# Kernel tuning notes

Measured on AMD Instinct MI355X. Metric: run time of the kernel, lower is better.

Reference implementation:

```python
import jax, jax.numpy as jnp
import numpy as np

STRIDE = 16
HF = WF = 160
IM_H = IM_W = STRIDE * HF  # 2560
A = 15
PRE_NMS = 3000
RPN_KEEP = 300
RPN_NMS_TH = 0.7
OBJ_TH = 0.2
MIN_SIZE = 8.0
G = 7
OUT_DIM = 10
S = 2  # bilinear samples per bin per axis
NUM_FG = 3
SCORE_TH = 0.3
RCNN_NMS_TH = 0.5
FINAL_KEEP = 100
BBOX_STD = jnp.array([0.1, 0.1, 0.2, 0.2], jnp.float32)


def gen_anchors():
    base = 16.0
    anchors = []
    for r in [0.5, 1.0, 2.0]:
        for s in [2.0, 4.0, 8.0, 16.0, 32.0]:
            size = base * s
            w = size * np.sqrt(1.0 / r)
            h = size * np.sqrt(r)
            anchors.append([-w / 2, -h / 2, w / 2, h / 2])
    return jnp.asarray(np.array(anchors, np.float32))  # [A,4]


def decode_boxes(anchors, deltas):
    d = deltas * BBOX_STD
    wa = anchors[..., 2] - anchors[..., 0] + 1.0
    ha = anchors[..., 3] - anchors[..., 1] + 1.0
    cxa = anchors[..., 0] + 0.5 * wa
    cya = anchors[..., 1] + 0.5 * ha
    cx = d[..., 0] * wa + cxa
    cy = d[..., 1] * ha + cya
    w = wa * jnp.exp(jnp.minimum(d[..., 2], 4.0))
    h = ha * jnp.exp(jnp.minimum(d[..., 3], 4.0))
    boxes = jnp.stack([cx - 0.5 * w, cy - 0.5 * h, cx + 0.5 * w, cy + 0.5 * h], -1)
    hi = jnp.array([IM_W - 1.0, IM_H - 1.0, IM_W - 1.0, IM_H - 1.0], jnp.float32)
    return jnp.clip(boxes, 0.0, hi)


def greedy_nms(boxes, scores, iou_th, keep_n):
    # scores <= 0 means pre-suppressed/invalid
    N = boxes.shape[0]
    areas = jnp.maximum(boxes[:, 2] - boxes[:, 0] + 1.0, 0.0) * jnp.maximum(boxes[:, 3] - boxes[:, 1] + 1.0, 0.0)

    def body(k, st):
        sup, keep = st
        s = jnp.where(sup, -1e30, scores)
        i = jnp.argmax(s)
        valid = s[i] > -1e29
        keep = keep.at[k].set(jnp.where(valid, i.astype(jnp.int32), N))
        bi = boxes[i]
        ix1 = jnp.maximum(bi[0], boxes[:, 0]); iy1 = jnp.maximum(bi[1], boxes[:, 1])
        ix2 = jnp.minimum(bi[2], boxes[:, 2]); iy2 = jnp.minimum(bi[3], boxes[:, 3])
        inter = jnp.maximum(ix2 - ix1 + 1.0, 0.0) * jnp.maximum(iy2 - iy1 + 1.0, 0.0)
        iou = inter / jnp.maximum(areas[i] + areas - inter, 1e-6)
        sup2 = (sup | (iou > iou_th)).at[i].set(True)
        sup = jnp.where(valid, sup2, sup)
        return sup, keep

    sup0 = scores <= 0.0
    keep0 = jnp.full((keep_n,), N, jnp.int32)
    _, keep = jax.lax.fori_loop(0, keep_n, body, (sup0, keep0))
    return keep, keep < N


def rpn_proposal(rpn_cls, rpn_bbox):
    fg = rpn_cls[0, A:]                                           # [A,HF,WF] objectness
    deltas = rpn_bbox[0].reshape(A, 4, HF, WF).transpose(0, 2, 3, 1)  # [A,HF,WF,4]
    anchors = gen_anchors()
    sx = jnp.arange(WF, dtype=jnp.float32) * STRIDE
    sy = jnp.arange(HF, dtype=jnp.float32) * STRIDE
    gx, gy = jnp.meshgrid(sx, sy)                                 # [HF,WF]
    shift = jnp.stack([gx, gy, gx, gy], -1)                       # [HF,WF,4]
    all_anchors = anchors[:, None, None, :] + shift[None]         # [A,HF,WF,4]
    boxes = decode_boxes(all_anchors, deltas).reshape(-1, 4)      # [A*HF*WF,4]
    scores = fg.reshape(-1)
    w = boxes[:, 2] - boxes[:, 0] + 1.0
    h = boxes[:, 3] - boxes[:, 1] + 1.0
    ok = (w >= MIN_SIZE) & (h >= MIN_SIZE) & (scores > OBJ_TH)
    scores = jnp.where(ok, scores, 0.0)
    sc, idx = jax.lax.top_k(scores, PRE_NMS)
    bx = boxes[idx]
    keep, valid = greedy_nms(bx, sc, RPN_NMS_TH, RPN_KEEP)
    bxp = jnp.concatenate([bx, jnp.zeros((1, 4), bx.dtype)], 0)
    rois = bxp[keep] * valid[:, None].astype(bx.dtype)            # [RPN_KEEP,4]
    return rois, valid


def psroi_align(ft, rois, valid):
    # ft [490,HF,WF]; position-sensitive channel = (c*G+ph)*G+pw
    x1 = rois[:, 0] / STRIDE; y1 = rois[:, 1] / STRIDE
    x2 = rois[:, 2] / STRIDE; y2 = rois[:, 3] / STRIDE
    bw = jnp.maximum(x2 - x1, 0.1) / G
    bh = jnp.maximum(y2 - y1, 0.1) / G
    frac = (jnp.arange(S, dtype=jnp.float32) + 0.5) / S           # [S]
    grid = jnp.arange(G, dtype=jnp.float32)[None, :, None] + frac[None, None, :]  # [1,G,S]
    ys = jnp.clip(y1[:, None, None] + grid * bh[:, None, None], 0.0, HF - 1.0)    # [R,G,S]
    xs = jnp.clip(x1[:, None, None] + grid * bw[:, None, None], 0.0, WF - 1.0)
    y0 = jnp.floor(ys); x0 = jnp.floor(xs)
    wy = ys - y0; wx = xs - x0
    y0i = y0.astype(jnp.int32); x0i = x0.astype(jnp.int32)
    y1i = jnp.minimum(y0i + 1, HF - 1); x1i = jnp.minimum(x0i + 1, WF - 1)
    chan = (jnp.arange(OUT_DIM)[:, None, None] * G + jnp.arange(G)[None, :, None]) * G + jnp.arange(G)[None, None, :]
    ch = chan[None, :, :, :, None, None]                          # [1,C,G,G,1,1]
    Y0 = y0i[:, None, :, None, :, None]; Y1 = y1i[:, None, :, None, :, None]
    X0 = x0i[:, None, None, :, None, :]; X1 = x1i[:, None, None, :, None, :]
    WY = wy[:, None, :, None, :, None]; WX = wx[:, None, None, :, None, :]
    v00 = ft[ch, Y0, X0]; v01 = ft[ch, Y0, X1]
    v10 = ft[ch, Y1, X0]; v11 = ft[ch, Y1, X1]                    # [R,C,G,G,S,S]
    val = v00 * (1 - WY) * (1 - WX) + v01 * (1 - WY) * WX + v10 * WY * (1 - WX) + v11 * WY * WX
    pooled = val.mean(axis=(4, 5))                                # [R,C,G,G]
    return pooled * valid[:, None, None, None].astype(pooled.dtype)


def rcnn_proposal(cls_sm, bbox_pred, rois, valid):
    R = rois.shape[0]
    deltas = bbox_pred.reshape(R, 4, 4)[:, 1:, :]                 # [R,3,4] fg classes
    boxes = decode_boxes(rois[:, None, :], deltas)                # [R,3,4]
    scores = cls_sm[:, 1:] * valid[:, None].astype(cls_sm.dtype)  # [R,3]
    scores = jnp.where(scores > SCORE_TH, scores, 0.0)
    fb = boxes.reshape(-1, 4)
    fs = scores.reshape(-1)
    labels = jnp.tile(jnp.arange(1, NUM_FG + 1, dtype=jnp.float32), (R,))
    keep, kv = greedy_nms(fb, fs, RCNN_NMS_TH, FINAL_KEEP)
    fbp = jnp.concatenate([fb, jnp.zeros((1, 4), fb.dtype)], 0)
    fsp = jnp.concatenate([fs, jnp.zeros((1,), fs.dtype)], 0)
    flp = jnp.concatenate([labels, jnp.zeros((1,), labels.dtype)], 0)
    out = jnp.concatenate([fbp[keep], fsp[keep][:, None], flp[keep][:, None]], -1)  # [FINAL_KEEP,6]
    return out * kv[:, None].astype(out.dtype)


def setup_inputs() -> dict:
    key = jax.random.key(0)
    ks = jax.random.split(key, 9)
    return {
        'rpn_cls_prob_reshape': jax.random.uniform(ks[0], (1, 2 * A, HF, WF), jnp.float32),
        'rpn_bbox_pred': jax.random.normal(ks[1], (1, 4 * A, HF, WF), jnp.float32),
        'ft_add_left_right': jax.random.normal(ks[2], (1, OUT_DIM * G * G, HF, WF), jnp.float32),
        'w1': jax.random.normal(ks[3], (490, 2048), jnp.float32) * 0.02,
        'b1': jnp.zeros((2048,), jnp.float32),
        'w_cls': jax.random.normal(ks[4], (2048, 4), jnp.float32) * 0.02,
        'b_cls': jnp.zeros((4,), jnp.float32),
        'w_bbox': jax.random.normal(ks[5], (2048, 16), jnp.float32) * 0.02,
        'b_bbox': jnp.zeros((16,), jnp.float32),
    }


def reference(rpn_cls_prob_reshape, rpn_bbox_pred, ft_add_left_right, w1, b1, w_cls, b_cls, w_bbox, b_bbox):
    rois, valid = rpn_proposal(rpn_cls_prob_reshape, rpn_bbox_pred)
    pooled = psroi_align(ft_add_left_right[0], rois, valid)       # [R,10,7,7]
    feats = pooled.reshape(-1, OUT_DIM * G * G)                   # [R,490]
    h = jax.nn.relu(feats @ w1 + b1)
    cls_sm = jax.nn.softmax(h @ w_cls + b_cls, axis=-1)
    bbox = h @ w_bbox + b_bbox
    return rcnn_proposal(cls_sm, bbox, rois, valid)
```

## Files before the change

### kernel.cpp

```cpp
#include <hip/hip_runtime.h>
#include <stdint.h>

#define HF_ 160
#define WF_ 160
#define HFW 25600
#define A_N 15
#define NTOT 384000
#define PRE_N 3000
#define KEEP_N 300
#define FEAT_N 490
#define HID_N 2048
#define RC_N 900
#define FIN_N 100
#define TIE_CAP 1024
#define NW 47
#define NSTAGE 384
#define RNW 15
#define FC1_MT 10
#define FC1_KP 496

__constant__ float c_hw[15] = {
  22.627416997969522f, 45.254833995939045f, 90.509667991878090f, 181.01933598375618f, 362.03867196751236f,
  16.0f, 32.0f, 64.0f, 128.0f, 256.0f,
  11.313708498984761f, 22.627416997969522f, 45.254833995939045f, 90.509667991878090f, 181.01933598375618f
};
__constant__ float c_hh[15] = {
  11.313708498984761f, 22.627416997969522f, 45.254833995939045f, 90.509667991878090f, 181.01933598375618f,
  16.0f, 32.0f, 64.0f, 128.0f, 256.0f,
  22.627416997969522f, 45.254833995939045f, 90.509667991878090f, 181.01933598375618f, 362.03867196751236f
};

__device__ __forceinline__ void decode_one(
    float ax1, float ay1, float ax2, float ay2,
    float dx, float dy, float dw, float dh,
    float& ox1, float& oy1, float& ox2, float& oy2)
{
#pragma clang fp contract(off)
  float wa = (ax2 - ax1) + 1.0f;
  float ha = (ay2 - ay1) + 1.0f;
  float cxa = ax1 + 0.5f * wa;
  float cya = ay1 + 0.5f * ha;
  float d0 = dx * 0.1f;
  float d1 = dy * 0.1f;
  float d2 = dw * 0.2f;
  float d3 = dh * 0.2f;
  float cx = d0 * wa + cxa;
  float cy = d1 * ha + cya;
  float w  = wa * expf(fminf(d2, 4.0f));
  float h  = ha * expf(fminf(d3, 4.0f));
  float x1 = cx - 0.5f * w;
  float y1 = cy - 0.5f * h;
  float x2 = cx + 0.5f * w;
  float y2 = cy + 0.5f * h;
  ox1 = fminf(fmaxf(x1, 0.0f), 2559.0f);
  oy1 = fminf(fmaxf(y1, 0.0f), 2559.0f);
  ox2 = fminf(fmaxf(x2, 0.0f), 2559.0f);
  oy2 = fminf(fmaxf(y2, 0.0f), 2559.0f);
}

__device__ __forceinline__ float iou_ref(
    float ax1, float ay1, float ax2, float ay2, float areaA,
    float bx1, float by1, float bx2, float by2)
{
#pragma clang fp contract(off)
  float ix1 = fmaxf(ax1, bx1);
  float iy1 = fmaxf(ay1, by1);
  float ix2 = fminf(ax2, bx2);
  float iy2 = fminf(ay2, by2);
  float iw = fmaxf((ix2 - ix1) + 1.0f, 0.0f);
  float ih = fmaxf((iy2 - iy1) + 1.0f, 0.0f);
  float inter = iw * ih;
  float areaB = fmaxf((bx2 - bx1) + 1.0f, 0.0f) * fmaxf((by2 - by1) + 1.0f, 0.0f);
  float den = fmaxf(areaA + areaB - inter, 1e-6f);
  return inter / den;
}

__global__ void k_zero(uint32_t* __restrict__ p, int n)
{
  int i = blockIdx.x * 256 + threadIdx.x;
  if (i < n) p[i] = 0u;
}

__global__ void k_decode_score(const float* __restrict__ cls,
                               const float* __restrict__ bbox,
                               float* __restrict__ scores)
{
  int e = blockIdx.x * 256 + threadIdx.x;
  if (e >= NTOT) return;
  int a   = e / HFW;
  int rem = e - a * HFW;
  int i   = rem / WF_;
  int j   = rem - i * WF_;
  float score = cls[(A_N + a) * HFW + rem];
  float gx = (float)(j * 16);
  float gy = (float)(i * 16);
  float hw = c_hw[a], hh = c_hh[a];
  float dx = bbox[(a * 4 + 0) * HFW + rem];
  float dy = bbox[(a * 4 + 1) * HFW + rem];
  float dw = bbox[(a * 4 + 2) * HFW + rem];
  float dh = bbox[(a * 4 + 3) * HFW + rem];
  float x1, y1, x2, y2;
  decode_one(gx - hw, gy - hh, gx + hw, gy + hh, dx, dy, dw, dh, x1, y1, x2, y2);
  float bw, bh;
  {
#pragma clang fp contract(off)
    bw = (x2 - x1) + 1.0f;
    bh = (y2 - y1) + 1.0f;
  }
  bool ok = (bw >= 8.0f) && (bh >= 8.0f) && (score > 0.2f);
  scores[e] = ok ? score : 0.0f;
}

__global__ void k_hist_hi(const float* __restrict__ scores, uint32_t* __restrict__ hist)
{
  __shared__ uint32_t lh[512];
  int t = threadIdx.x;
  for (int i = t; i < 512; i += 256) lh[i] = 0u;
  __syncthreads();
  int e = blockIdx.x * 256 + t;
  if (e < NTOT) {
    float s = scores[e];
    if (s > 0.0f) {
      uint32_t b = __float_as_uint(s) >> 16;
      if (b >= 0x3E00u && b < 0x4000u) atomicAdd(&lh[b - 0x3E00u], 1u);
      else atomicAdd(&hist[b], 1u);
    }
  }
  __syncthreads();
  for (int i = t; i < 512; i += 256) {
    uint32_t v = lh[i];
    if (v) atomicAdd(&hist[0x3E00u + i], v);
  }
}

__global__ void __launch_bounds__(1024) k_findbin1(const uint32_t* __restrict__ hist,
                                                   uint32_t* __restrict__ meta)
{
  __shared__ uint32_t sfx[1024];
  __shared__ int s_chunk;
  __shared__ uint32_t s_exc;
  int t = threadIdx.x;
  if (t == 0) s_chunk = -1;
  const uint32_t* hp = hist + t * 64;
  uint32_t s = 0;
#pragma unroll
  for (int b = 0; b < 64; b++) s += hp[b];
  sfx[t] = s;
  __syncthreads();
  for (int d = 1; d < 1024; d <<= 1) {
    uint32_t v = (t + d < 1024) ? sfx[t + d] : 0u;
    __syncthreads();
    sfx[t] += v;
    __syncthreads();
  }
  uint32_t inc = sfx[t];
  uint32_t exc = (t < 1023) ? sfx[t + 1] : 0u;
  if (exc < (uint32_t)PRE_N && inc >= (uint32_t)PRE_N) { s_chunk = t; s_exc = exc; }
  __syncthreads();
  int c = s_chunk;
  if (c < 0) {
    if (t == 0) { meta[0] = 0u; meta[1] = 0u; meta[2] = 1u; }
    return;
  }
  if (t < 64) {
    uint32_t h = hist[c * 64 + t];
    uint32_t v = h;
#pragma unroll
    for (int d = 1; d < 64; d <<= 1) {
      uint32_t o = (uint32_t)__shfl_down((int)v, d);
      v += (t + d < 64) ? o : 0u;
    }
    uint32_t before = s_exc + (v - h);
    if (before < (uint32_t)PRE_N && before + h >= (uint32_t)PRE_N) {
      meta[0] = (uint32_t)(c * 64 + t);
      meta[1] = (uint32_t)PRE_N - before;
      meta[2] = 0u;
    }
  }
}

__global__ void k_hist_lo(const float* __restrict__ scores,
                          const uint32_t* __restrict__ meta,
                          uint32_t* __restrict__ hist2)
{
  if (meta[2]) return;
  uint32_t B1 = meta[0];
  int e = blockIdx.x * 256 + threadIdx.x;
  if (e >= NTOT) return;
  float s = scores[e];
  if (s <= 0.0f) return;
  uint32_t bits = __float_as_uint(s);
  if ((bits >> 16) == B1) atomicAdd(&hist2[bits & 0xFFFFu], 1u);
}

__global__ void __launch_bounds__(1024) k_findT(const uint32_t* __restrict__ hist2,
                                                uint32_t* __restrict__ meta)
{
  if (meta[2]) { if (threadIdx.x == 0) meta[3] = 0u; return; }
  __shared__ uint32_t sfx[1024];
  __shared__ int s_chunk;
  __shared__ uint32_t s_exc;
  int t = threadIdx.x;
  if (t == 0) s_chunk = -1;
  uint32_t K = meta[1];
  const uint32_t* hp = hist2 + t * 64;
  uint32_t s = 0;
#pragma unroll
  for (int b = 0; b < 64; b++) s += hp[b];
  sfx[t] = s;
  __syncthreads();
  for (int d = 1; d < 1024; d <<= 1) {
    uint32_t v = (t + d < 1024) ? sfx[t + d] : 0u;
    __syncthreads();
    sfx[t] += v;
    __syncthreads();
  }
  uint32_t inc = sfx[t];
  uint32_t exc = (t < 1023) ? sfx[t + 1] : 0u;
  if (exc < K && inc >= K) { s_chunk = t; s_exc = exc; }
  __syncthreads();
  int c = s_chunk;
  if (c < 0) { if (t == 0) meta[3] = 0u; return; }
  if (t < 64) {
    uint32_t h = hist2[c * 64 + t];
    uint32_t v = h;
#pragma unroll
    for (int d = 1; d < 64; d <<= 1) {
      uint32_t o = (uint32_t)__shfl_down((int)v, d);
      v += (t + d < 64) ? o : 0u;
    }
    uint32_t before = s_exc + (v - h);
    if (before < K && before + h >= K)
      meta[3] = (meta[0] << 16) | (uint32_t)(c * 64 + t);
  }
}

__global__ void k_compact(const float* __restrict__ scores,
                          const uint32_t* __restrict__ meta,
                          uint64_t* __restrict__ gt,
                          uint64_t* __restrict__ tie,
                          uint32_t* __restrict__ cnts)
{
  int e = blockIdx.x * 256 + threadIdx.x;
  if (e >= NTOT) return;
  float s = scores[e];
  if (s <= 0.0f) return;
  uint32_t bits = __float_as_uint(s);
  uint32_t T = meta[3];
  uint64_t key = ((uint64_t)bits << 32) | (uint32_t)(~(uint32_t)e);
  if (bits > T) {
    uint32_t p = atomicAdd(&cnts[0], 1u);
    if (p < (uint32_t)PRE_N) gt[p] = key;
  } else if (bits == T) {
    uint32_t p = atomicAdd(&cnts[1], 1u);
    if (p < (uint32_t)TIE_CAP) tie[p] = key;
  }
}

__global__ void __launch_bounds__(1024) k_sort(const uint64_t* __restrict__ gt,
                                               const uint64_t* __restrict__ tie,
                                               const uint32_t* __restrict__ cnts,
                                               int* __restrict__ top_idx)
{
  __shared__ uint64_t key[4096];
  int t = threadIdx.x;
  uint32_t ngt = min(cnts[0], (uint32_t)PRE_N);
  uint32_t nte = min(cnts[1], (uint32_t)TIE_CAP);
  for (int s = t; s < 4096; s += 1024) {
    uint64_t k = 0;
    if ((uint32_t)s < ngt) k = gt[s];
    else if ((uint32_t)s < ngt + nte) k = tie[s - ngt];
    key[s] = k;
  }
  for (unsigned size = 2; size <= 4096; size <<= 1) {
    for (unsigned stride = size >> 1; stride > 0; stride >>= 1) {
      __syncthreads();
      for (unsigned i = t; i < 4096; i += 1024) {
        unsigned p = i ^ stride;
        if (p > i) {
          bool desc = ((i & size) == 0);
          uint64_t a = key[i], b = key[p];
          if (desc ? (a < b) : (a > b)) { key[i] = b; key[p] = a; }
        }
      }
    }
  }
  __syncthreads();
  for (int s = t; s < PRE_N; s += 1024) {
    uint64_t k = key[s];
    top_idx[s] = (int)(~(uint32_t)(k & 0xFFFFFFFFull));
  }
}

__global__ void k_gather(const int* __restrict__ top_idx,
                         const float* __restrict__ bbox,
                         float* __restrict__ bxx1, float* __restrict__ bxy1,
                         float* __restrict__ bxx2, float* __restrict__ bxy2)
{
  int s = blockIdx.x * 256 + threadIdx.x;
  if (s >= PRE_N) return;
  int idx = top_idx[s];
  float x1 = 0.f, y1 = 0.f, x2 = 0.f, y2 = 0.f;
  if (idx >= 0) {
    int a   = idx / HFW;
    int rem = idx - a * HFW;
    int i   = rem / WF_;
    int j   = rem - i * WF_;
    float gx = (float)(j * 16);
    float gy = (float)(i * 16);
    float hw = c_hw[a], hh = c_hh[a];
    float dx = bbox[(a * 4 + 0) * HFW + rem];
    float dy = bbox[(a * 4 + 1) * HFW + rem];
    float dw = bbox[(a * 4 + 2) * HFW + rem];
    float dh = bbox[(a * 4 + 3) * HFW + rem];
    decode_one(gx - hw, gy - hh, gx + hw, gy + hh, dx, dy, dw, dh, x1, y1, x2, y2);
  }
  bxx1[s] = x1; bxy1[s] = y1; bxx2[s] = x2; bxy2[s] = y2;
}

__global__ void __launch_bounds__(256) k_iou_mask(
    const float* __restrict__ bxx1, const float* __restrict__ bxy1,
    const float* __restrict__ bxx2, const float* __restrict__ bxy2,
    uint64_t* __restrict__ rowmask)
{
  __shared__ float s1[PRE_N], s2[PRE_N], s3[PRE_N], s4[PRE_N];
  int t = threadIdx.x;
  for (int e = t; e < PRE_N; e += 256) {
    s1[e] = bxx1[e]; s2[e] = bxy1[e]; s3[e] = bxx2[e]; s4[e] = bxy2[e];
  }
  __syncthreads();
  int task = blockIdx.x * 256 + t;
  if (task >= PRE_N * NW) return;
  int row = task / NW;
  int w   = task - row * NW;
  float ax1 = s1[row], ay1 = s2[row], ax2 = s3[row], ay2 = s4[row];
  float areaA;
  {
#pragma clang fp contract(off)
    areaA = fmaxf((ax2 - ax1) + 1.0f, 0.0f) * fmaxf((ay2 - ay1) + 1.0f, 0.0f);
  }
  int j0 = w << 6;
  uint64_t bits = 0;
  for (int off = 0; off < 64; off++) {
    int jj = (off + t) & 63;
    int j = j0 + jj;
    if (j < PRE_N) {
      float iou = iou_ref(ax1, ay1, ax2, ay2, areaA, s1[j], s2[j], s3[j], s4[j]);
      if (iou > 0.7f) bits |= 1ull << jj;
    }
  }
  rowmask[(size_t)row * NW + w] = bits;
}

__global__ void __launch_bounds__(256) k_rpn_scan(
    const float* __restrict__ bxx1, const float* __restrict__ bxy1,
    const float* __restrict__ bxx2, const float* __restrict__ bxy2,
    const uint32_t* __restrict__ cnts,
    const uint64_t* __restrict__ rowmask,
    float* __restrict__ rois, uint32_t* __restrict__ valid)
{
  __shared__ uint64_t rowstage[NSTAGE * NW];
  __shared__ int keepIdx[KEEP_N];
  __shared__ int s_nkeep;
  int t = threadIdx.x;
  for (int e = t; e < NSTAGE * NW; e += 256) rowstage[e] = rowmask[e];
  __syncthreads();
  if (t < 64) {
    int lane = t;
    uint32_t Mp = min(cnts[0] + min(cnts[1], (uint32_t)TIE_CAP), (uint32_t)PRE_N);
    uint64_t sup = 0, cw = 0;
    int nk = 0;
    for (uint32_t i = 0; i < Mp && nk < KEEP_N; i++) {
      uint32_t b = i & 63u;
      if (((cw >> b) & 1ull) == 0ull) {
        uint64_t row = 0;
        if (lane < NW)
          row = (i < NSTAGE) ? rowstage[i * NW + lane]
                             : rowmask[(size_t)i * NW + lane];
        sup |= row;
        cw |= (uint64_t)__shfl((unsigned long long)row, (int)(i >> 6));
        if (lane == 0) keepIdx[nk] = (int)i;
        nk++;
      }
      if (b == 63u) cw = (uint64_t)__shfl((unsigned long long)sup, (int)(i >> 6) + 1);
    }
    if (lane == 0) s_nkeep = nk;
  }
  __syncthreads();
  int nk2 = s_nkeep;
  for (int k = t; k < nk2; k += 256) {
    int i = keepIdx[k];
    rois[k * 4 + 0] = bxx1[i];
    rois[k * 4 + 1] = bxy1[i];
    rois[k * 4 + 2] = bxx2[i];
    rois[k * 4 + 3] = bxy2[i];
    valid[k] = 1u;
  }
  for (int e = nk2 * 4 + t; e < KEEP_N * 4; e += 256) rois[e] = 0.0f;
  for (int e = nk2 + t; e < KEEP_N; e += 256) valid[e] = 0u;
}

__global__ void __launch_bounds__(512) k_psroi(const float* __restrict__ ft,
                                               const float* __restrict__ rois,
                                               const uint32_t* __restrict__ valid,
                                               float* __restrict__ feats)
{
#pragma clang fp contract(off)
  int r = blockIdx.x;
  int t = threadIdx.x;
  if (t >= FEAT_N) return;
  float x1 = rois[r * 4 + 0] * 0.0625f;
  float y1 = rois[r * 4 + 1] * 0.0625f;
  float x2 = rois[r * 4 + 2] * 0.0625f;
  float y2 = rois[r * 4 + 3] * 0.0625f;
  float bw = fmaxf(x2 - x1, 0.1f) / 7.0f;
  float bh = fmaxf(y2 - y1, 0.1f) / 7.0f;
  int c   = t / 49;
  int rem = t - c * 49;
  int gy  = rem / 7;
  int gx  = rem - gy * 7;
  (void)c;
  const float* base = ft + t * HFW;
  float acc = 0.0f;
  for (int sy = 0; sy < 2; sy++) {
    float gyf = (float)gy + (sy ? 0.75f : 0.25f);
    float ys = fminf(fmaxf(y1 + gyf * bh, 0.0f), 159.0f);
    float y0f = floorf(ys);
    float wy = ys - y0f;
    int y0 = (int)y0f;
    int y1i = min(y0 + 1, 159);
    for (int sx = 0; sx < 2; sx++) {
      float gxf = (float)gx + (sx ? 0.75f : 0.25f);
      float xs = fminf(fmaxf(x1 + gxf * bw, 0.0f), 159.0f);
      float x0f = floorf(xs);
      float wx = xs - x0f;
      int x0 = (int)x0f;
      int x1i = min(x0 + 1, 159);
      float v00 = base[y0 * WF_ + x0];
      float v01 = base[y0 * WF_ + x1i];
      float v10 = base[y1i * WF_ + x0];
      float v11 = base[y1i * WF_ + x1i];
      float val = v00 * (1.0f - wy) * (1.0f - wx)
                + v01 * (1.0f - wy) * wx
                + v10 * wy * (1.0f - wx)
                + v11 * wy * wx;
      acc += val;
    }
  }
  float pooled = acc * 0.25f;
  feats[r * FEAT_N + t] = valid[r] ? pooled : 0.0f;
}

__global__ void __launch_bounds__(256) k_fc1(const float* __restrict__ feats,
                                             const float* __restrict__ w1,
                                             const float* __restrict__ b1,
                                             float* __restrict__ h)
{
  __shared__ float sf[FC1_MT][FC1_KP];
  int t = threadIdx.x;
  int n = blockIdx.x * 256 + t;
  int m0 = blockIdx.y * FC1_MT;
  for (int idx = t; idx < FC1_MT * FC1_KP; idx += 256) {
    int mm = idx / FC1_KP;
    int kk = idx - mm * FC1_KP;
    sf[mm][kk] = (kk < FEAT_N) ? feats[(m0 + mm) * FEAT_N + kk] : 0.0f;
  }
  __syncthreads();
  float acc[FC1_MT];
#pragma unroll
  for (int i = 0; i < FC1_MT; i++) acc[i] = 0.0f;
  float wb[16];
#pragma unroll
  for (int u = 0; u < 16; u++) wb[u] = w1[u * HID_N + n];
#pragma unroll 1
  for (int kb = 0; kb < FC1_KP - 16; kb += 16) {
    float wn[16];
    int kn = kb + 16;
#pragma unroll
    for (int u = 0; u < 16; u++)
      wn[u] = (kn + u < FEAT_N) ? w1[(kn + u) * HID_N + n] : 0.0f;
#pragma unroll
    for (int u4 = 0; u4 < 4; u4++) {
#pragma unroll
      for (int i = 0; i < FC1_MT; i++) {
        float4 f = *reinterpret_cast<const float4*>(&sf[i][kb + u4 * 4]);
        acc[i] = fmaf(f.x, wb[u4 * 4 + 0], acc[i]);
        acc[i] = fmaf(f.y, wb[u4 * 4 + 1], acc[i]);
        acc[i] = fmaf(f.z, wb[u4 * 4 + 2], acc[i]);
        acc[i] = fmaf(f.w, wb[u4 * 4 + 3], acc[i]);
      }
    }
#pragma unroll
    for (int u = 0; u < 16; u++) wb[u] = wn[u];
  }
  {
    const int kb = FC1_KP - 16;
#pragma unroll
    for (int u4 = 0; u4 < 4; u4++) {
#pragma unroll
      for (int i = 0; i < FC1_MT; i++) {
        float4 f = *reinterpret_cast<const float4*>(&sf[i][kb + u4 * 4]);
        acc[i] = fmaf(f.x, wb[u4 * 4 + 0], acc[i]);
        acc[i] = fmaf(f.y, wb[u4 * 4 + 1], acc[i]);
        acc[i] = fmaf(f.z, wb[u4 * 4 + 2], acc[i]);
        acc[i] = fmaf(f.w, wb[u4 * 4 + 3], acc[i]);
      }
    }
  }
  float b = b1[n];
#pragma unroll
  for (int i = 0; i < FC1_MT; i++) h[(m0 + i) * HID_N + n] = fmaxf(acc[i] + b, 0.0f);
}

__global__ void __launch_bounds__(256) k_fc2(const float* __restrict__ h,
                                             const float* __restrict__ w_cls,
                                             const float* __restrict__ b_cls,
                                             const float* __restrict__ w_bbox,
                                             const float* __restrict__ b_bbox,
                                             const uint32_t* __restrict__ valid,
                                             float* __restrict__ scores3,
                                             float* __restrict__ bbox16)
{
  int r = blockIdx.x;
  int t = threadIdx.x;
  float acc[20];
#pragma unroll
  for (int i = 0; i < 20; i++) acc[i] = 0.0f;
  for (int k = t; k < HID_N; k += 256) {
    float hv = h[r * HID_N + k];
    float4 wc = *reinterpret_cast<const float4*>(w_cls + k * 4);
    acc[0] = fmaf(hv, wc.x, acc[0]);
    acc[1] = fmaf(hv, wc.y, acc[1]);
    acc[2] = fmaf(hv, wc.z, acc[2]);
    acc[3] = fmaf(hv, wc.w, acc[3]);
#pragma unroll
    for (int q = 0; q < 4; q++) {
      float4 wb = *reinterpret_cast<const float4*>(w_bbox + k * 16 + q * 4);
      acc[4 + q * 4 + 0] = fmaf(hv, wb.x, acc[4 + q * 4 + 0]);
      acc[4 + q * 4 + 1] = fmaf(hv, wb.y, acc[4 + q * 4 + 1]);
      acc[4 + q * 4 + 2] = fmaf(hv, wb.z, acc[4 + q * 4 + 2]);
      acc[4 + q * 4 + 3] = fmaf(hv, wb.w, acc[4 + q * 4 + 3]);
    }
  }
#pragma unroll
  for (int off = 32; off > 0; off >>= 1) {
#pragma unroll
    for (int i = 0; i < 20; i++) acc[i] += __shfl_down(acc[i], off);
  }
  __shared__ float red[4][20];
  int wid = t >> 6, lane = t & 63;
  if (lane == 0) {
#pragma unroll
    for (int i = 0; i < 20; i++) red[wid][i] = acc[i];
  }
  __syncthreads();
  if (t == 0) {
    float f[20];
#pragma unroll
    for (int i = 0; i < 20; i++) f[i] = red[0][i] + red[1][i] + red[2][i] + red[3][i];
    float l0 = f[0] + b_cls[0];
    float l1 = f[1] + b_cls[1];
    float l2 = f[2] + b_cls[2];
    float l3 = f[3] + b_cls[3];
    float m = fmaxf(fmaxf(l0, l1), fmaxf(l2, l3));
    float e0 = expf(l0 - m), e1 = expf(l1 - m), e2 = expf(l2 - m), e3 = expf(l3 - m);
    float s = ((e0 + e1) + e2) + e3;
    float vf = valid[r] ? 1.0f : 0.0f;
    scores3[r * 3 + 0] = (e1 / s) * vf;
    scores3[r * 3 + 1] = (e2 / s) * vf;
    scores3[r * 3 + 2] = (e3 / s) * vf;
#pragma unroll
    for (int i = 0; i < 16; i++) bbox16[r * 16 + i] = f[4 + i] + b_bbox[i];
  }
}

__global__ void k_rcnn_decode(const float* __restrict__ rois,
                              const float* __restrict__ scores3,
                              const float* __restrict__ bbox16,
                              float* __restrict__ fx1, float* __restrict__ fy1,
                              float* __restrict__ fx2, float* __restrict__ fy2,
                              float* __restrict__ fs)
{
  int e = blockIdx.x * 256 + threadIdx.x;
  if (e >= RC_N) return;
  int r = e / 3;
  int c = e - r * 3;
  float ax1 = rois[r * 4 + 0], ay1 = rois[r * 4 + 1];
  float ax2 = rois[r * 4 + 2], ay2 = rois[r * 4 + 3];
  int cb = (c + 1) * 4;
  float dx = bbox16[r * 16 + cb + 0];
  float dy = bbox16[r * 16 + cb + 1];
  float dw = bbox16[r * 16 + cb + 2];
  float dh = bbox16[r * 16 + cb + 3];
  float x1, y1, x2, y2;
  decode_one(ax1, ay1, ax2, ay2, dx, dy, dw, dh, x1, y1, x2, y2);
  fx1[e] = x1; fy1[e] = y1; fx2[e] = x2; fy2[e] = y2;
  float sc = scores3[e];
  fs[e] = (sc > 0.3f) ? sc : 0.0f;
}

__global__ void __launch_bounds__(1024) k_rc_sort(
    const float* __restrict__ fx1, const float* __restrict__ fy1,
    const float* __restrict__ fx2, const float* __restrict__ fy2,
    const float* __restrict__ fs,
    float* __restrict__ sx1, float* __restrict__ sy1,
    float* __restrict__ sx2, float* __restrict__ sy2,
    float* __restrict__ ssc, int* __restrict__ sidx,
    uint32_t* __restrict__ rc_meta)
{
  __shared__ uint64_t key[1024];
  int t = threadIdx.x;
  uint64_t k = 0;
  if (t < RC_N) {
    float sc = fs[t];
    if (sc > 0.0f)
      k = ((uint64_t)__float_as_uint(sc) << 32) | (uint32_t)(~(uint32_t)t);
  }
  key[t] = k;
  for (unsigned size = 2; size <= 1024; size <<= 1) {
    for (unsigned stride = size >> 1; stride > 0; stride >>= 1) {
      __syncthreads();
      unsigned p = t ^ stride;
      if (p > (unsigned)t) {
        bool desc = ((t & size) == 0);
        uint64_t a = key[t], b = key[p];
        if (desc ? (a < b) : (a > b)) { key[t] = b; key[p] = a; }
      }
    }
  }
  __syncthreads();
  uint64_t kk = key[t];
  if ((kk == 0) && (t == 0 || key[t - 1] != 0)) rc_meta[0] = (uint32_t)t;
  if (t < RC_N) {
    int m = (int)(~(uint32_t)(kk & 0xFFFFFFFFull));
    sidx[t] = m;
    ssc[t] = __uint_as_float((uint32_t)(kk >> 32));
    float a = 0.f, b = 0.f, c = 0.f, d = 0.f;
    if (m >= 0) { a = fx1[m]; b = fy1[m]; c = fx2[m]; d = fy2[m]; }
    sx1[t] = a; sy1[t] = b; sx2[t] = c; sy2[t] = d;
  }
}

__global__ void __launch_bounds__(256) k_rc_mask(
    const float* __restrict__ sx1, const float* __restrict__ sy1,
    const float* __restrict__ sx2, const float* __restrict__ sy2,
    uint64_t* __restrict__ rcmask)
{
  __shared__ float s1[RC_N], s2[RC_N], s3[RC_N], s4[RC_N];
  int t = threadIdx.x;
  for (int e = t; e < RC_N; e += 256) {
    s1[e] = sx1[e]; s2[e] = sy1[e]; s3[e] = sx2[e]; s4[e] = sy2[e];
  }
  __syncthreads();
  int task = blockIdx.x * 256 + t;
  if (task >= RC_N * RNW) return;
  int row = task / RNW;
  int w   = task - row * RNW;
  float ax1 = s1[row], ay1 = s2[row], ax2 = s3[row], ay2 = s4[row];
  float areaA;
  {
#pragma clang fp contract(off)
    areaA = fmaxf((ax2 - ax1) + 1.0f, 0.0f) * fmaxf((ay2 - ay1) + 1.0f, 0.0f);
  }
  int j0 = w << 6;
  uint64_t bits = 0;
  for (int off = 0; off < 64; off++) {
    int jj = (off + t) & 63;
    int j = j0 + jj;
    if (j < RC_N) {
      float iou = iou_ref(ax1, ay1, ax2, ay2, areaA, s1[j], s2[j], s3[j], s4[j]);
      if (iou > 0.5f) bits |= 1ull << jj;
    }
  }
  rcmask[(size_t)row * RNW + w] = bits;
}

__global__ void __launch_bounds__(256) k_rc_scan(
    const float* __restrict__ sx1, const float* __restrict__ sy1,
    const float* __restrict__ sx2, const float* __restrict__ sy2,
    const float* __restrict__ ssc, const int* __restrict__ sidx,
    const uint32_t* __restrict__ rc_meta,
    const uint64_t* __restrict__ rcmask,
    float* __restrict__ out)
{
  __shared__ uint64_t rowstage[RC_N * RNW];
  __shared__ int keepPos[FIN_N];
  __shared__ int s_nk;
  int t = threadIdx.x;
  for (int e = t; e < RC_N * RNW; e += 256) rowstage[e] = rcmask[e];
  __syncthreads();
  if (t < 64) {
    int lane = t;
    int Npos = (int)min(rc_meta[0], (uint32_t)RC_N);
    uint64_t sup = 0, cw = 0;
    int nk = 0;
    for (int i = 0; i < Npos && nk < FIN_N; i++) {
      int b = i & 63;
      if (((cw >> b) & 1ull) == 0ull) {
        uint64_t row = (lane < RNW) ? rowstage[i * RNW + lane] : 0;
        sup |= row;
        cw |= (uint64_t)__shfl((unsigned long long)row, i >> 6);
        if (lane == 0) keepPos[nk] = i;
        nk++;
      }
      if (b == 63) cw = (uint64_t)__shfl((unsigned long long)sup, (i >> 6) + 1);
    }
    if (lane == 0) s_nk = nk;
  }
  __syncthreads();
  int nk = s_nk;
  for (int k = t; k < nk; k += 256) {
    int i = keepPos[k];
    int m = sidx[i];
    out[k * 6 + 0] = sx1[i];
    out[k * 6 + 1] = sy1[i];
    out[k * 6 + 2] = sx2[i];
    out[k * 6 + 3] = sy2[i];
    out[k * 6 + 4] = ssc[i];
    out[k * 6 + 5] = (float)(m - (m / 3) * 3 + 1);
  }
  for (int e = nk * 6 + t; e < FIN_N * 6; e += 256) out[e] = 0.0f;
}

extern "C" void kernel_launch(void* const* d_in, const int* in_sizes, int n_in,
                              void* d_out, int out_size, void* d_ws, size_t ws_size,
                              hipStream_t stream)
{
  (void)in_sizes; (void)n_in; (void)out_size; (void)ws_size;
  const float* rpn_cls  = (const float*)d_in[0];
  const float* rpn_bbox = (const float*)d_in[1];
  const float* ft       = (const float*)d_in[2];
  const float* w1       = (const float*)d_in[3];
  const float* b1       = (const float*)d_in[4];
  const float* w_cls    = (const float*)d_in[5];
  const float* b_cls    = (const float*)d_in[6];
  const float* w_bbox   = (const float*)d_in[7];
  const float* b_bbox   = (const float*)d_in[8];
  float* out = (float*)d_out;

  char* ws = (char*)d_ws;
  size_t off = 0;
  auto alloc = [&](size_t bytes) -> void* {
    void* p = (void*)(ws + off);
    off += (bytes + 15) & ~(size_t)15;
    return p;
  };
  uint32_t* hist1  = (uint32_t*)alloc(65536 * 4);
  uint32_t* hist2  = (uint32_t*)alloc(65536 * 4);
  uint32_t* meta   = (uint32_t*)alloc(32 * 4);
  float*    scores = (float*)alloc((size_t)NTOT * 4);
  uint64_t* gt     = (uint64_t*)alloc(3008 * 8);
  uint64_t* tie    = (uint64_t*)alloc(TIE_CAP * 8);
  int*      top_idx = (int*)alloc(PRE_N * 4);
  float*    bxx1 = (float*)alloc(PRE_N * 4);
  float*    bxy1 = (float*)alloc(PRE_N * 4);
  float*    bxx2 = (float*)alloc(PRE_N * 4);
  float*    bxy2 = (float*)alloc(PRE_N * 4);
  float*    rois  = (float*)alloc(KEEP_N * 4 * 4);
  uint32_t* valid = (uint32_t*)alloc(KEEP_N * 4);
  float*    feats = (float*)alloc((size_t)KEEP_N * FEAT_N * 4);
  float*    hbuf  = (float*)alloc((size_t)KEEP_N * HID_N * 4);
  float*    scores3 = (float*)alloc(RC_N * 4);
  float*    bbox16  = (float*)alloc(KEEP_N * 16 * 4);
  float*    fx1 = (float*)alloc(RC_N * 4);
  float*    fy1 = (float*)alloc(RC_N * 4);
  float*    fx2 = (float*)alloc(RC_N * 4);
  float*    fy2 = (float*)alloc(RC_N * 4);
  float*    fsb = (float*)alloc(RC_N * 4);
  float*    sx1 = (float*)alloc(RC_N * 4);
  float*    sy1 = (float*)alloc(RC_N * 4);
  float*    sx2 = (float*)alloc(RC_N * 4);
  float*    sy2 = (float*)alloc(RC_N * 4);
  float*    ssc = (float*)alloc(RC_N * 4);
  int*      sidx = (int*)alloc(RC_N * 4);
  uint32_t* rc_meta = (uint32_t*)alloc(16 * 4);
  uint64_t* rowmask = (uint64_t*)alloc((size_t)3008 * NW * 8);
  uint64_t* rcmask  = (uint64_t*)alloc((size_t)RC_N * RNW * 8);

  const int ZN = 65536 * 2 + 32;
  k_zero<<<(ZN + 255) / 256, 256, 0, stream>>>(hist1, ZN);
  k_decode_score<<<NTOT / 256, 256, 0, stream>>>(rpn_cls, rpn_bbox, scores);
  k_hist_hi<<<NTOT / 256, 256, 0, stream>>>(scores, hist1);
  k_findbin1<<<1, 1024, 0, stream>>>(hist1, meta);
  k_hist_lo<<<NTOT / 256, 256, 0, stream>>>(scores, meta, hist2);
  k_findT<<<1, 1024, 0, stream>>>(hist2, meta);
  k_compact<<<NTOT / 256, 256, 0, stream>>>(scores, meta, gt, tie, meta + 8);
  k_sort<<<1, 1024, 0, stream>>>(gt, tie, meta + 8, top_idx);
  k_gather<<<(PRE_N + 255) / 256, 256, 0, stream>>>(top_idx, rpn_bbox,
                                                    bxx1, bxy1, bxx2, bxy2);
  k_iou_mask<<<(PRE_N * NW + 255) / 256, 256, 0, stream>>>(bxx1, bxy1, bxx2, bxy2, rowmask);
  k_rpn_scan<<<1, 256, 0, stream>>>(bxx1, bxy1, bxx2, bxy2, meta + 8, rowmask, rois, valid);
  k_psroi<<<KEEP_N, 512, 0, stream>>>(ft, rois, valid, feats);
  k_fc1<<<dim3(HID_N / 256, KEEP_N / FC1_MT), 256, 0, stream>>>(feats, w1, b1, hbuf);
  k_fc2<<<KEEP_N, 256, 0, stream>>>(hbuf, w_cls, b_cls, w_bbox, b_bbox, valid,
                                    scores3, bbox16);
  k_rcnn_decode<<<(RC_N + 255) / 256, 256, 0, stream>>>(rois, scores3, bbox16,
                                                        fx1, fy1, fx2, fy2, fsb);
  k_rc_sort<<<1, 1024, 0, stream>>>(fx1, fy1, fx2, fy2, fsb,
                                    sx1, sy1, sx2, sy2, ssc, sidx, rc_meta);
  k_rc_mask<<<(RC_N * RNW + 255) / 256, 256, 0, stream>>>(sx1, sy1, sx2, sy2, rcmask);
  k_rc_scan<<<1, 256, 0, stream>>>(sx1, sy1, sx2, sy2, ssc, sidx, rc_meta, rcmask, out);
}
```

Baseline: 472.1 us.

## Fuse small kernels and rewrite NMS scans to skip suppressed candidates via diagonal masks

Measured after the change: 470.4 us. Within noise of the previous version (-0.4%).

```diff
diff --git a/kernel.cpp b/kernel.cpp
--- a/kernel.cpp
+++ b/kernel.cpp
@@ -14,10 +14,11 @@
 #define FIN_N 100
 #define TIE_CAP 1024
 #define NW 47
-#define NSTAGE 384
+#define NSTAGE 320
 #define RNW 15
 #define FC1_MT 10
 #define FC1_KP 496
+#define ZN (65536 * 2 + 32)
 
 __constant__ float c_hw[15] = {
   22.627416997969522f, 45.254833995939045f, 90.509667991878090f, 181.01933598375618f, 362.03867196751236f,
@@ -75,17 +76,13 @@
   return inter / den;
 }
 
-__global__ void k_zero(uint32_t* __restrict__ p, int n)
-{
-  int i = blockIdx.x * 256 + threadIdx.x;
-  if (i < n) p[i] = 0u;
-}
-
 __global__ void k_decode_score(const float* __restrict__ cls,
                                const float* __restrict__ bbox,
-                               float* __restrict__ scores)
+                               float* __restrict__ scores,
+                               uint32_t* __restrict__ histzero)
 {
   int e = blockIdx.x * 256 + threadIdx.x;
+  if (e < ZN) histzero[e] = 0u;
   if (e >= NTOT) return;
   int a   = e / HFW;
   int rem = e - a * HFW;
@@ -257,10 +254,13 @@
   }
 }
 
-__global__ void __launch_bounds__(1024) k_sort(const uint64_t* __restrict__ gt,
-                                               const uint64_t* __restrict__ tie,
-                                               const uint32_t* __restrict__ cnts,
-                                               int* __restrict__ top_idx)
+__global__ void __launch_bounds__(1024) k_sort_gather(
+    const uint64_t* __restrict__ gt,
+    const uint64_t* __restrict__ tie,
+    const uint32_t* __restrict__ cnts,
+    const float* __restrict__ bbox,
+    float* __restrict__ bxx1, float* __restrict__ bxy1,
+    float* __restrict__ bxx2, float* __restrict__ bxy2)
 {
   __shared__ uint64_t key[4096];
   int t = threadIdx.x;
@@ -288,40 +288,30 @@
   __syncthreads();
   for (int s = t; s < PRE_N; s += 1024) {
     uint64_t k = key[s];
-    top_idx[s] = (int)(~(uint32_t)(k & 0xFFFFFFFFull));
-  }
-}
-
-__global__ void k_gather(const int* __restrict__ top_idx,
-                         const float* __restrict__ bbox,
-                         float* __restrict__ bxx1, float* __restrict__ bxy1,
-                         float* __restrict__ bxx2, float* __restrict__ bxy2)
-{
-  int s = blockIdx.x * 256 + threadIdx.x;
-  if (s >= PRE_N) return;
-  int idx = top_idx[s];
-  float x1 = 0.f, y1 = 0.f, x2 = 0.f, y2 = 0.f;
-  if (idx >= 0) {
-    int a   = idx / HFW;
-    int rem = idx - a * HFW;
-    int i   = rem / WF_;
-    int j   = rem - i * WF_;
-    float gx = (float)(j * 16);
-    float gy = (float)(i * 16);
-    float hw = c_hw[a], hh = c_hh[a];
-    float dx = bbox[(a * 4 + 0) * HFW + rem];
-    float dy = bbox[(a * 4 + 1) * HFW + rem];
-    float dw = bbox[(a * 4 + 2) * HFW + rem];
-    float dh = bbox[(a * 4 + 3) * HFW + rem];
-    decode_one(gx - hw, gy - hh, gx + hw, gy + hh, dx, dy, dw, dh, x1, y1, x2, y2);
-  }
-  bxx1[s] = x1; bxy1[s] = y1; bxx2[s] = x2; bxy2[s] = y2;
+    int idx = (int)(~(uint32_t)(k & 0xFFFFFFFFull));
+    float x1 = 0.f, y1 = 0.f, x2 = 0.f, y2 = 0.f;
+    if (idx >= 0) {
+      int a   = idx / HFW;
+      int rem = idx - a * HFW;
+      int i   = rem / WF_;
+      int j   = rem - i * WF_;
+      float gx = (float)(j * 16);
+      float gy = (float)(i * 16);
+      float hw = c_hw[a], hh = c_hh[a];
+      float dx = bbox[(a * 4 + 0) * HFW + rem];
+      float dy = bbox[(a * 4 + 1) * HFW + rem];
+      float dw = bbox[(a * 4 + 2) * HFW + rem];
+      float dh = bbox[(a * 4 + 3) * HFW + rem];
+      decode_one(gx - hw, gy - hh, gx + hw, gy + hh, dx, dy, dw, dh, x1, y1, x2, y2);
+    }
+    bxx1[s] = x1; bxy1[s] = y1; bxx2[s] = x2; bxy2[s] = y2;
+  }
 }
 
 __global__ void __launch_bounds__(256) k_iou_mask(
     const float* __restrict__ bxx1, const float* __restrict__ bxy1,
     const float* __restrict__ bxx2, const float* __restrict__ bxy2,
-    uint64_t* __restrict__ rowmask)
+    uint64_t* __restrict__ rowmask, uint64_t* __restrict__ diag)
 {
   __shared__ float s1[PRE_N], s2[PRE_N], s3[PRE_N], s4[PRE_N];
   int t = threadIdx.x;
@@ -333,6 +323,10 @@
   if (task >= PRE_N * NW) return;
   int row = task / NW;
   int w   = task - row * NW;
+  if ((w + 1) * 64 <= row) {
+    rowmask[(size_t)row * NW + w] = 0;
+    return;
+  }
   float ax1 = s1[row], ay1 = s2[row], ax2 = s3[row], ay2 = s4[row];
   float areaA;
   {
@@ -350,6 +344,7 @@
     }
   }
   rowmask[(size_t)row * NW + w] = bits;
+  if (w == (row >> 6)) diag[row] = bits;
 }
 
 __global__ void __launch_bounds__(256) k_rpn_scan(
@@ -357,33 +352,45 @@
     const float* __restrict__ bxx2, const float* __restrict__ bxy2,
     const uint32_t* __restrict__ cnts,
     const uint64_t* __restrict__ rowmask,
+    const uint64_t* __restrict__ diag,
     float* __restrict__ rois, uint32_t* __restrict__ valid)
 {
   __shared__ uint64_t rowstage[NSTAGE * NW];
+  __shared__ uint64_t sdiag[PRE_N];
   __shared__ int keepIdx[KEEP_N];
   __shared__ int s_nkeep;
   int t = threadIdx.x;
   for (int e = t; e < NSTAGE * NW; e += 256) rowstage[e] = rowmask[e];
+  for (int e = t; e < PRE_N; e += 256) sdiag[e] = diag[e];
   __syncthreads();
   if (t < 64) {
     int lane = t;
     uint32_t Mp = min(cnts[0] + min(cnts[1], (uint32_t)TIE_CAP), (uint32_t)PRE_N);
-    uint64_t sup = 0, cw = 0;
+    uint64_t sup = 0, pend = 0;
     int nk = 0;
-    for (uint32_t i = 0; i < Mp && nk < KEEP_N; i++) {
-      uint32_t b = i & 63u;
-      if (((cw >> b) & 1ull) == 0ull) {
-        uint64_t row = 0;
+    int nwords = (int)((Mp + 63u) >> 6);
+    for (int w = 0; w < nwords && nk < KEEP_N; w++) {
+      sup |= pend; pend = 0;
+      uint64_t cw = (uint64_t)__shfl((unsigned long long)sup, w);
+      int lim = (int)Mp - (w << 6);
+      uint64_t range = (lim >= 64) ? ~0ull : ((1ull << lim) - 1ull);
+      uint64_t rem = (~cw) & range;
+      while (rem && nk < KEEP_N) {
+        int b = __builtin_ctzll(rem);
+        int i = (w << 6) + b;
+        if (lane == 0) keepIdx[nk] = i;
+        nk++;
+        uint64_t roww = sdiag[i];
+        uint64_t rowl = 0;
         if (lane < NW)
-          row = (i < NSTAGE) ? rowstage[i * NW + lane]
-                             : rowmask[(size_t)i * NW + lane];
-        sup |= row;
-        cw |= (uint64_t)__shfl((unsigned long long)row, (int)(i >> 6));
-        if (lane == 0) keepIdx[nk] = (int)i;
-        nk++;
+          rowl = (i < NSTAGE) ? rowstage[i * NW + lane]
+                              : rowmask[(size_t)i * NW + lane];
+        sup |= pend;
+        pend = rowl;
+        rem &= ~(roww | (1ull << b));
       }
-      if (b == 63u) cw = (uint64_t)__shfl((unsigned long long)sup, (int)(i >> 6) + 1);
-    }
+    }
+    sup |= pend;
     if (lane == 0) s_nkeep = nk;
   }
   __syncthreads();
@@ -574,46 +581,34 @@
   }
 }
 
-__global__ void k_rcnn_decode(const float* __restrict__ rois,
-                              const float* __restrict__ scores3,
-                              const float* __restrict__ bbox16,
-                              float* __restrict__ fx1, float* __restrict__ fy1,
-                              float* __restrict__ fx2, float* __restrict__ fy2,
-                              float* __restrict__ fs)
-{
-  int e = blockIdx.x * 256 + threadIdx.x;
-  if (e >= RC_N) return;
-  int r = e / 3;
-  int c = e - r * 3;
-  float ax1 = rois[r * 4 + 0], ay1 = rois[r * 4 + 1];
-  float ax2 = rois[r * 4 + 2], ay2 = rois[r * 4 + 3];
-  int cb = (c + 1) * 4;
-  float dx = bbox16[r * 16 + cb + 0];
-  float dy = bbox16[r * 16 + cb + 1];
-  float dw = bbox16[r * 16 + cb + 2];
-  float dh = bbox16[r * 16 + cb + 3];
-  float x1, y1, x2, y2;
-  decode_one(ax1, ay1, ax2, ay2, dx, dy, dw, dh, x1, y1, x2, y2);
-  fx1[e] = x1; fy1[e] = y1; fx2[e] = x2; fy2[e] = y2;
-  float sc = scores3[e];
-  fs[e] = (sc > 0.3f) ? sc : 0.0f;
-}
-
-__global__ void __launch_bounds__(1024) k_rc_sort(
-    const float* __restrict__ fx1, const float* __restrict__ fy1,
-    const float* __restrict__ fx2, const float* __restrict__ fy2,
-    const float* __restrict__ fs,
+__global__ void __launch_bounds__(1024) k_rc_sortdec(
+    const float* __restrict__ rois,
+    const float* __restrict__ scores3,
+    const float* __restrict__ bbox16,
     float* __restrict__ sx1, float* __restrict__ sy1,
     float* __restrict__ sx2, float* __restrict__ sy2,
     float* __restrict__ ssc, int* __restrict__ sidx,
     uint32_t* __restrict__ rc_meta)
 {
   __shared__ uint64_t key[1024];
+  __shared__ float bx[RC_N], by[RC_N], bX[RC_N], bY[RC_N];
   int t = threadIdx.x;
   uint64_t k = 0;
   if (t < RC_N) {
-    float sc = fs[t];
-    if (sc > 0.0f)
+    int r = t / 3;
+    int c = t - r * 3;
+    float ax1 = rois[r * 4 + 0], ay1 = rois[r * 4 + 1];
+    float ax2 = rois[r * 4 + 2], ay2 = rois[r * 4 + 3];
+    int cb = (c + 1) * 4;
+    float dx = bbox16[r * 16 + cb + 0];
+    float dy = bbox16[r * 16 + cb + 1];
+    float dw = bbox16[r * 16 + cb + 2];
+    float dh = bbox16[r * 16 + cb + 3];
+    float x1, y1, x2, y2;
+    decode_one(ax1, ay1, ax2, ay2, dx, dy, dw, dh, x1, y1, x2, y2);
+    bx[t] = x1; by[t] = y1; bX[t] = x2; bY[t] = y2;
+    float sc = scores3[t];
+    if (sc > 0.3f)
       k = ((uint64_t)__float_as_uint(sc) << 32) | (uint32_t)(~(uint32_t)t);
   }
   key[t] = k;
@@ -636,7 +631,7 @@
     sidx[t] = m;
     ssc[t] = __uint_as_float((uint32_t)(kk >> 32));
     float a = 0.f, b = 0.f, c = 0.f, d = 0.f;
-    if (m >= 0) { a = fx1[m]; b = fy1[m]; c = fx2[m]; d = fy2[m]; }
+    if (m >= 0) { a = bx[m]; b = by[m]; c = bX[m]; d = bY[m]; }
     sx1[t] = a; sy1[t] = b; sx2[t] = c; sy2[t] = d;
   }
 }
@@ -644,7 +639,7 @@
 __global__ void __launch_bounds__(256) k_rc_mask(
     const float* __restrict__ sx1, const float* __restrict__ sy1,
     const float* __restrict__ sx2, const float* __restrict__ sy2,
-    uint64_t* __restrict__ rcmask)
+    uint64_t* __restrict__ rcmask, uint64_t* __restrict__ rcdiag)
 {
   __shared__ float s1[RC_N], s2[RC_N], s3[RC_N], s4[RC_N];
   int t = threadIdx.x;
@@ -656,6 +651,10 @@
   if (task >= RC_N * RNW) return;
   int row = task / RNW;
   int w   = task - row * RNW;
+  if ((w + 1) * 64 <= row) {
+    rcmask[(size_t)row * RNW + w] = 0;
+    return;
+  }
   float ax1 = s1[row], ay1 = s2[row], ax2 = s3[row], ay2 = s4[row];
   float areaA;
   {
@@ -673,6 +672,7 @@
     }
   }
   rcmask[(size_t)row * RNW + w] = bits;
+  if (w == (row >> 6)) rcdiag[row] = bits;
 }
 
 __global__ void __launch_bounds__(256) k_rc_scan(
@@ -681,30 +681,42 @@
     const float* __restrict__ ssc, const int* __restrict__ sidx,
     const uint32_t* __restrict__ rc_meta,
     const uint64_t* __restrict__ rcmask,
+    const uint64_t* __restrict__ rcdiag,
     float* __restrict__ out)
 {
   __shared__ uint64_t rowstage[RC_N * RNW];
+  __shared__ uint64_t sdiag[RC_N];
   __shared__ int keepPos[FIN_N];
   __shared__ int s_nk;
   int t = threadIdx.x;
   for (int e = t; e < RC_N * RNW; e += 256) rowstage[e] = rcmask[e];
+  for (int e = t; e < RC_N; e += 256) sdiag[e] = rcdiag[e];
   __syncthreads();
   if (t < 64) {
     int lane = t;
     int Npos = (int)min(rc_meta[0], (uint32_t)RC_N);
-    uint64_t sup = 0, cw = 0;
+    uint64_t sup = 0, pend = 0;
     int nk = 0;
-    for (int i = 0; i < Npos && nk < FIN_N; i++) {
-      int b = i & 63;
-      if (((cw >> b) & 1ull) == 0ull) {
-        uint64_t row = (lane < RNW) ? rowstage[i * RNW + lane] : 0;
-        sup |= row;
-        cw |= (uint64_t)__shfl((unsigned long long)row, i >> 6);
+    int nwords = (Npos + 63) >> 6;
+    for (int w = 0; w < nwords && nk < FIN_N; w++) {
+      sup |= pend; pend = 0;
+      uint64_t cw = (uint64_t)__shfl((unsigned long long)sup, w);
+      int lim = Npos - (w << 6);
+      uint64_t range = (lim >= 64) ? ~0ull : ((1ull << lim) - 1ull);
+      uint64_t rem = (~cw) & range;
+      while (rem && nk < FIN_N) {
+        int b = __builtin_ctzll(rem);
+        int i = (w << 6) + b;
         if (lane == 0) keepPos[nk] = i;
         nk++;
+        uint64_t roww = sdiag[i];
+        uint64_t rowl = (lane < RNW) ? rowstage[i * RNW + lane] : 0;
+        sup |= pend;
+        pend = rowl;
+        rem &= ~(roww | (1ull << b));
       }
-      if (b == 63) cw = (uint64_t)__shfl((unsigned long long)sup, (i >> 6) + 1);
-    }
+    }
+    sup |= pend;
     if (lane == 0) s_nk = nk;
   }
   __syncthreads();
@@ -751,7 +763,6 @@
   float*    scores = (float*)alloc((size_t)NTOT * 4);
   uint64_t* gt     = (uint64_t*)alloc(3008 * 8);
   uint64_t* tie    = (uint64_t*)alloc(TIE_CAP * 8);
-  int*      top_idx = (int*)alloc(PRE_N * 4);
   float*    bxx1 = (float*)alloc(PRE_N * 4);
   float*    bxy1 = (float*)alloc(PRE_N * 4);
   float*    bxx2 = (float*)alloc(PRE_N * 4);
@@ -762,11 +773,6 @@
   float*    hbuf  = (float*)alloc((size_t)KEEP_N * HID_N * 4);
   float*    scores3 = (float*)alloc(RC_N * 4);
   float*    bbox16  = (float*)alloc(KEEP_N * 16 * 4);
-  float*    fx1 = (float*)alloc(RC_N * 4);
-  float*    fy1 = (float*)alloc(RC_N * 4);
-  float*    fx2 = (float*)alloc(RC_N * 4);
-  float*    fy2 = (float*)alloc(RC_N * 4);
-  float*    fsb = (float*)alloc(RC_N * 4);
   float*    sx1 = (float*)alloc(RC_N * 4);
   float*    sy1 = (float*)alloc(RC_N * 4);
   float*    sx2 = (float*)alloc(RC_N * 4);
@@ -775,29 +781,30 @@
   int*      sidx = (int*)alloc(RC_N * 4);
   uint32_t* rc_meta = (uint32_t*)alloc(16 * 4);
   uint64_t* rowmask = (uint64_t*)alloc((size_t)3008 * NW * 8);
+  uint64_t* diag    = (uint64_t*)alloc(3008 * 8);
   uint64_t* rcmask  = (uint64_t*)alloc((size_t)RC_N * RNW * 8);
-
-  const int ZN = 65536 * 2 + 32;
-  k_zero<<<(ZN + 255) / 256, 256, 0, stream>>>(hist1, ZN);
-  k_decode_score<<<NTOT / 256, 256, 0, stream>>>(rpn_cls, rpn_bbox, scores);
+  uint64_t* rcdiag  = (uint64_t*)alloc(904 * 8);
+
+  k_decode_score<<<NTOT / 256, 256, 0, stream>>>(rpn_cls, rpn_bbox, scores, hist1);
   k_hist_hi<<<NTOT / 256, 256, 0, stream>>>(scores, hist1);
   k_findbin1<<<1, 1024, 0, stream>>>(hist1, meta);
   k_hist_lo<<<NTOT / 256, 256, 0, stream>>>(scores, meta, hist2);
   k_findT<<<1, 1024, 0, stream>>>(hist2, meta);
   k_compact<<<NTOT / 256, 256, 0, stream>>>(scores, meta, gt, tie, meta + 8);
-  k_sort<<<1, 1024, 0, stream>>>(gt, tie, meta + 8, top_idx);
-  k_gather<<<(PRE_N + 255) / 256, 256, 0, stream>>>(top_idx, rpn_bbox,
-                                                    bxx1, bxy1, bxx2, bxy2);
-  k_iou_mask<<<(PRE_N * NW + 255) / 256, 256, 0, stream>>>(bxx1, bxy1, bxx2, bxy2, rowmask);
-  k_rpn_scan<<<1, 256, 0, stream>>>(bxx1, bxy1, bxx2, bxy2, meta + 8, rowmask, rois, valid);
+  k_sort_gather<<<1, 1024, 0, stream>>>(gt, tie, meta + 8, rpn_bbox,
+                                        bxx1, bxy1, bxx2, bxy2);
+  k_iou_mask<<<(PRE_N * NW + 255) / 256, 256, 0, stream>>>(bxx1, bxy1, bxx2, bxy2,
+                                                           rowmask, diag);
+  k_rpn_scan<<<1, 256, 0, stream>>>(bxx1, bxy1, bxx2, bxy2, meta + 8,
+                                    rowmask, diag, rois, valid);
   k_psroi<<<KEEP_N, 512, 0, stream>>>(ft, rois, valid, feats);
   k_fc1<<<dim3(HID_N / 256, KEEP_N / FC1_MT), 256, 0, stream>>>(feats, w1, b1, hbuf);
   k_fc2<<<KEEP_N, 256, 0, stream>>>(hbuf, w_cls, b_cls, w_bbox, b_bbox, valid,
                                     scores3, bbox16);
-  k_rcnn_decode<<<(RC_N + 255) / 256, 256, 0, stream>>>(rois, scores3, bbox16,
-                                                        fx1, fy1, fx2, fy2, fsb);
-  k_rc_sort<<<1, 1024, 0, stream>>>(fx1, fy1, fx2, fy2, fsb,
-                                    sx1, sy1, sx2, sy2, ssc, sidx, rc_meta);
-  k_rc_mask<<<(RC_N * RNW + 255) / 256, 256, 0, stream>>>(sx1, sy1, sx2, sy2, rcmask);
-  k_rc_scan<<<1, 256, 0, stream>>>(sx1, sy1, sx2, sy2, ssc, sidx, rc_meta, rcmask, out);
-}
+  k_rc_sortdec<<<1, 1024, 0, stream>>>(rois, scores3, bbox16,
+                                       sx1, sy1, sx2, sy2, ssc, sidx, rc_meta);
+  k_rc_mask<<<(RC_N * RNW + 255) / 256, 256, 0, stream>>>(sx1, sy1, sx2, sy2,
+                                                          rcmask, rcdiag);
+  k_rc_scan<<<1, 256, 0, stream>>>(sx1, sy1, sx2, sy2, ssc, sidx, rc_meta,
+                                   rcmask, rcdiag, out);
+}
```
